# Kernel tuning notes

Measured on AMD Instinct MI355X. Metric: run time of the kernel, lower is better.

## Reference

```python
import jax, jax.numpy as jnp
import numpy as np

N = 50000
NEG_SLOPE = 0.01  # F.leaky_relu default


def gcn_conv(x, edge_index, edge_weight, W, b):
    """PyG GCNConv: h = x @ W; symmetric-normalized aggregation with self-loops; + bias."""
    n = x.shape[0]
    h = x @ W                                # [N, out]
    src, dst = edge_index[0], edge_index[1]
    # degree includes self-loop weight 1.0 per node
    deg = jax.ops.segment_sum(edge_weight, dst, num_segments=n) + 1.0
    dinv = jax.lax.rsqrt(deg)                # deg >= 1, no zero guard needed
    norm = dinv[src] * edge_weight * dinv[dst]
    agg = jax.ops.segment_sum(norm[:, None] * h[src], dst, num_segments=n)
    agg = agg + (dinv * dinv)[:, None] * h   # self-loop contribution: deg^-1 * h_i
    return agg + b


def setup_inputs() -> dict:
    key = jax.random.key(0)
    ks = jax.random.split(key, 24)
    in_size, hid, out = 256, 64, 32
    E = 800000
    d = {}
    for i, nm in enumerate(["x1", "x2", "x3"]):
        d[nm] = jax.random.normal(ks[i], (N, in_size), dtype=jnp.float32)
    for i, nm in enumerate(["edge_index1", "edge_index2", "edge_index3"]):
        d[nm] = jax.random.randint(ks[3 + i], (2, E), 0, N, dtype=jnp.int32)
    for i, nm in enumerate(["edge_weight1", "edge_weight2", "edge_weight3"]):
        d[nm] = jax.random.uniform(ks[6 + i], (E,), dtype=jnp.float32)
    s_in = 1.0 / np.sqrt(in_size)
    s_h = 1.0 / np.sqrt(hid)
    for i, nm in enumerate(["W1", "W2", "W3"]):
        d[nm] = jax.random.uniform(ks[9 + i], (in_size, hid), minval=-s_in, maxval=s_in, dtype=jnp.float32)
    for i, nm in enumerate(["b1", "b2", "b3"]):
        d[nm] = jax.random.uniform(ks[12 + i], (hid,), minval=-s_in, maxval=s_in, dtype=jnp.float32)
    d["fc_w"] = jax.random.uniform(ks[15], (hid, 1), minval=-s_h, maxval=s_h, dtype=jnp.float32)
    d["fc_b"] = jax.random.uniform(ks[16], (1,), minval=-s_h, maxval=s_h, dtype=jnp.float32)
    for i, nm in enumerate(["W11", "W22", "W33"]):
        d[nm] = jax.random.uniform(ks[17 + i], (hid, out), minval=-s_h, maxval=s_h, dtype=jnp.float32)
    for i, nm in enumerate(["b11", "b22", "b33"]):
        d[nm] = jax.random.uniform(ks[20 + i], (out,), minval=-s_h, maxval=s_h, dtype=jnp.float32)
    return d


def reference(x1, x2, x3, edge_index1, edge_index2, edge_index3,
              edge_weight1, edge_weight2, edge_weight3,
              W1, W2, W3, b1, b2, b3, fc_w, fc_b,
              W11, W22, W33, b11, b22, b33):
    # branch embeddings (dropout is identity in eval mode)
    e1 = jax.nn.relu(gcn_conv(x1, edge_index1, edge_weight1, W1, b1))
    e2 = jax.nn.relu(gcn_conv(x2, edge_index2, edge_weight2, W2, b2))
    e3 = jax.nn.relu(gcn_conv(x3, edge_index3, edge_weight3, W3, b3))
    # attention coefficients
    c1 = jnp.exp(jax.nn.leaky_relu(e1 @ fc_w + fc_b, NEG_SLOPE))  # [N,1]
    c2 = jnp.exp(jax.nn.leaky_relu(e2 @ fc_w + fc_b, NEG_SLOPE))
    c3 = jnp.exp(jax.nn.leaky_relu(e3 @ fc_w + fc_b, NEG_SLOPE))
    cd = c1 + c2 + c3
    coef1, coef2, coef3 = c1 / cd, c2 / cd, c3 / cd
    combined = e1 * coef1 + e2 * coef2 + e3 * coef3
    out1 = gcn_conv(combined, edge_index1, edge_weight1, W11, b11)
    out2 = gcn_conv(combined, edge_index2, edge_weight2, W22, b22)
    out3 = gcn_conv(combined, edge_index3, edge_weight3, W33, b33)
    return (out1 + out2 + out3, coef1, coef2, coef3)
```

## Files before the change

### kernel.cpp

```cpp
#include <hip/hip_runtime.h>
#include <hip/hip_fp16.h>
#include <math.h>

#define NN    50000
#define INF_  256
#define HID   64
#define OUTF  32
#define EE    800000
#define TOTN  (3 * NN)
#define NBKT  196
#define NBIN  (3 * NBKT)
#define CBLK  392
#define NCNT  (3 * CBLK)
#define GB    782
#define NGEMM (3 * GB)
#define MAXB  5120
#define NBLK  12500

typedef unsigned long long u64;
typedef unsigned int       u32;
typedef unsigned short     u16;
typedef _Float16           f16;
typedef f16   f16x8 __attribute__((ext_vector_type(8)));
typedef f16   f16x4 __attribute__((ext_vector_type(4)));
typedef float f32x4 __attribute__((ext_vector_type(4)));

__global__ __launch_bounds__(256) void k_prep(
        const float* __restrict__ W1, const float* __restrict__ W2, const float* __restrict__ W3,
        f16* __restrict__ Wt, u32* __restrict__ bin_total) {
    int blk = blockIdx.x, t = threadIdx.x;
    if (blk == 3) {
        for (int i = t; i < NBIN; i += 256) bin_total[i] = 0;
        return;
    }
    const float* W = (blk == 0) ? W1 : (blk == 1) ? W2 : W3;
    f16* wt = Wt + blk * HID * INF_;
    for (int idx = t; idx < INF_ * HID; idx += 256) {
        int k = idx >> 6, c = idx & 63;
        wt[c * INF_ + k] = (f16)W[idx];
    }
}

__global__ __launch_bounds__(256) void k_cntgemm(
        const int* __restrict__ ei1, const int* __restrict__ ei2, const int* __restrict__ ei3,
        u32* __restrict__ bin_total, u32* __restrict__ blockbase,
        const float* __restrict__ x1, const float* __restrict__ x2, const float* __restrict__ x3,
        const f16* __restrict__ Wt, __half* __restrict__ h) {
    __shared__ f16 xl[64][72];
    __shared__ f16 wl[64][72];
    int bid = blockIdx.x;
    int q = bid / 3, r = bid - q * 3;
    int t = threadIdx.x;

    if (r == 2) {
        u32* bins = (u32*)xl;
        int cb  = q;
        int br  = cb / CBLK;
        int blk = cb - br * CBLK;
        const int* ei = (br == 0) ? ei1 : (br == 1) ? ei2 : ei3;
        for (int i = t; i < NBKT; i += 256) bins[i] = 0;
        __syncthreads();
        int e0 = blk * 2048;
#pragma unroll
        for (int k = 0; k < 8; ++k) {
            int e = e0 + k * 256 + t;
            if (e < EE) atomicAdd(&bins[(u32)ei[EE + e] >> 8], 1u);
        }
        __syncthreads();
        for (int i = t; i < NBKT; i += 256) {
            u32 c = bins[i];
            u32 base = atomicAdd(&bin_total[br * NBKT + i], c);
            blockbase[cb * NBKT + i] = base;
        }
        return;
    }

    int gid = q * 2 + r;
    if (gid >= NGEMM) return;
    int b = gid / GB;
    int row_base = (gid - b * GB) * 64;
    const float4* x4 = reinterpret_cast<const float4*>((b == 0) ? x1 : (b == 1) ? x2 : x3);
    const f16* wt = Wt + b * HID * INF_;
    __half* hb = h + (size_t)b * NN * HID;

    int w    = t >> 6;
    int lane = t & 63;
    int lrow = lane & 15;
    int lk   = (lane >> 4) * 8;

    f32x4 acc[4] = {{0,0,0,0},{0,0,0,0},{0,0,0,0},{0,0,0,0}};
    for (int kt = 0; kt < 4; ++kt) {
#pragma unroll
        for (int j = 0; j < 4; ++j) {
            int flat = t + j * 256;
            int rr = flat >> 4, c4 = flat & 15;
            int gr = row_base + rr;
            float4 v = (gr < NN) ? x4[(size_t)gr * 64 + kt * 16 + c4]
                                 : make_float4(0.f, 0.f, 0.f, 0.f);
            f16x4 p = {(f16)v.x, (f16)v.y, (f16)v.z, (f16)v.w};
            *(f16x4*)&xl[rr][c4 * 4] = p;
        }
#pragma unroll
        for (int j = 0; j < 2; ++j) {
            int flat = t + j * 256;
            int col = flat >> 3, ko = (flat & 7) * 8;
            *(f16x8*)&wl[col][ko] = *(const f16x8*)&wt[col * INF_ + kt * 64 + ko];
        }
        __syncthreads();
        int arow = (w << 4) + lrow;
        f16x8 a0 = *(const f16x8*)&xl[arow][lk];
        f16x8 a1 = *(const f16x8*)&xl[arow][32 + lk];
#pragma unroll
        for (int c = 0; c < 4; ++c) {
            f16x8 b0 = *(const f16x8*)&wl[c * 16 + lrow][lk];
            f16x8 b1 = *(const f16x8*)&wl[c * 16 + lrow][32 + lk];
            acc[c] = __builtin_amdgcn_mfma_f32_16x16x32_f16(a0, b0, acc[c], 0, 0, 0);
            acc[c] = __builtin_amdgcn_mfma_f32_16x16x32_f16(a1, b1, acc[c], 0, 0, 0);
        }
        __syncthreads();
    }
    int orow0 = row_base + (w << 4) + ((lane >> 4) << 2);
#pragma unroll
    for (int c = 0; c < 4; ++c) {
#pragma unroll
        for (int i = 0; i < 4; ++i) {
            int row = orow0 + i;
            if (row < NN) hb[(size_t)row * HID + c * 16 + lrow] = __float2half(acc[c][i]);
        }
    }
}

__global__ __launch_bounds__(256) void k_scan(const u32* __restrict__ bin_total,
                                              u32* __restrict__ binstart) {
    __shared__ u32 s[256];
    int t = threadIdx.x;
    u32 c[3]; u32 sum = 0;
#pragma unroll
    for (int k = 0; k < 3; ++k) {
        int i = t * 3 + k;
        c[k] = (i < NBIN) ? bin_total[i] : 0;
        sum += c[k];
    }
    s[t] = sum;
    __syncthreads();
    for (int d = 1; d < 256; d <<= 1) {
        u32 v = (t >= d) ? s[t - d] : 0;
        __syncthreads();
        s[t] += v;
        __syncthreads();
    }
    u32 run = s[t] - sum;
#pragma unroll
    for (int k = 0; k < 3; ++k) {
        int i = t * 3 + k;
        if (i < NBIN) binstart[i] = run;
        run += c[k];
    }
    if (t == 255) binstart[NBIN] = run;
}

__global__ __launch_bounds__(256) void k_scatter(
        const int* __restrict__ ei1, const int* __restrict__ ei2, const int* __restrict__ ei3,
        const float* __restrict__ ew1, const float* __restrict__ ew2, const float* __restrict__ ew3,
        const u32* __restrict__ binstart, const u32* __restrict__ blockbase,
        u64* __restrict__ bucketed) {
    __shared__ u32 cur[NBKT];
    int cb  = blockIdx.x;
    int br  = cb / CBLK;
    int blk = cb - br * CBLK;
    const int*   ei = (br == 0) ? ei1 : (br == 1) ? ei2 : ei3;
    const float* ew = (br == 0) ? ew1 : (br == 1) ? ew2 : ew3;
    int t = threadIdx.x;
    for (int i = t; i < NBKT; i += 256) cur[i] = 0;
    __syncthreads();
    int e0 = blk * 2048;
#pragma unroll
    for (int k = 0; k < 8; ++k) {
        int e = e0 + k * 256 + t;
        if (e < EE) {
            u32 dst = (u32)ei[EE + e];
            u32 src = (u32)ei[e];
            u32 bkt = dst >> 8;
            u32 rnk = atomicAdd(&cur[bkt], 1u);
            u32 pos = binstart[br * NBKT + bkt] + blockbase[cb * NBKT + bkt] + rnk;
            bucketed[pos] = ((u64)__float_as_uint(ew[e]) << 32) | (src << 8) | (dst & 0xffu);
        }
    }
}

__global__ __launch_bounds__(256) void k_bucket(
        const u64* __restrict__ bucketed, const u32* __restrict__ bin_total,
        const u32* __restrict__ binstart,
        u32* __restrict__ nodeinfo, float* __restrict__ dinv,
        u32* __restrict__ csr, __half* __restrict__ h) {
    __shared__ u32   scnt[256];
    __shared__ float swsum[256];
    __shared__ u32   scur[256];
    __shared__ u32   sscan[256];
    __shared__ float sdiv[256];
    __shared__ u32   lcsr[MAXB];
    int bin = blockIdx.x;
    int br  = bin / NBKT;
    int bkt = bin - br * NBKT;
    int t = threadIdx.x;
    u32 base = binstart[bin];
    u32 ecnt = bin_total[bin];
    scnt[t] = 0; swsum[t] = 0.f; scur[t] = 0;
    __syncthreads();
    for (u32 i = t; i < ecnt; i += 256) {
        u64 e = bucketed[base + i];
        u32 dl = (u32)e & 0xffu;
        atomicAdd(&scnt[dl], 1u);
        atomicAdd(&swsum[dl], __uint_as_float((u32)(e >> 32)));
    }
    __syncthreads();
    sscan[t] = scnt[t];
    __syncthreads();
    for (int d = 1; d < 256; d <<= 1) {
        u32 v = (t >= d) ? sscan[t - d] : 0;
        __syncthreads();
        sscan[t] += v;
        __syncthreads();
    }
    u32 lstart = sscan[t] - scnt[t];
    float d = rsqrtf(1.0f + swsum[t]);
    sdiv[t] = d;
    int n = bkt * 256 + t;
    if (n < NN) {
        int gi = br * NN + n;
        nodeinfo[gi] = ((base + lstart) << 10) | scnt[t];
        dinv[gi]     = d;
    }
    __syncthreads();
    for (u32 i = t; i < ecnt; i += 256) {
        u64 e = bucketed[base + i];
        u32 dl  = (u32)e & 0xffu;
        u32 src = (u32)(e >> 8) & 0xffffu;
        float w = __uint_as_float((u32)(e >> 32));
        u32 rnk = atomicAdd(&scur[dl], 1u);
        u32 ls  = sscan[dl] - scnt[dl];
        lcsr[ls + rnk] = ((u32)__half_as_ushort(__float2half(w)) << 16) | src;
    }
    __syncthreads();
    for (u32 i = t; i < ecnt; i += 256) csr[base + i] = lcsr[i];

    int nrows = NN - bkt * 256; if (nrows > 256) nrows = 256;
    u32* hrow = (u32*)(h + ((size_t)br * NN + (size_t)bkt * 256) * HID);
    for (int i = t; i < nrows * 32; i += 256) {
        float dd = sdiv[i >> 5];
        __half2 hv = *(__half2*)&hrow[i];
        float2 v = __half22float2(hv);
        __half2 r = __float22half2_rn(make_float2(v.x * dd, v.y * dd));
        hrow[i] = *(u32*)&r;
    }
}

__global__ __launch_bounds__(256) void k_agg1(
        const u32* __restrict__ csr, const u32* __restrict__ nodeinfo,
        const float* __restrict__ dinv,
        const float* __restrict__ b1, const float* __restrict__ b2, const float* __restrict__ b3,
        const __half* __restrict__ h, __half* __restrict__ e) {
    int bid = blockIdx.x;
    int br  = bid / NBLK;
    int nb  = bid - br * NBLK;
    int t   = threadIdx.x;
    int f2  = t & 31;
    int eo  = (t >> 5) & 1;
    int sub = __builtin_amdgcn_readfirstlane(t >> 6);
    int n   = nb * 4 + sub;

    const float* bi = (br == 0) ? b1 : (br == 1) ? b2 : b3;
    const __half2* hb2 = (const __half2*)(h + (size_t)br * NN * HID);
    int i   = br * NN + n;
    u32 inf = nodeinfo[i];
    int cc  = (int)(inf & 1023u);
    int st  = (int)(inf >> 10);
    float d = dinv[i];
    float2 hs = __half22float2(hb2[(size_t)n * 32 + f2]);

    float ax = 0.f, ay = 0.f;
    int cm1 = cc - 1;
    for (int j = 0; j < cc; j += 16) {
        u32 ee[8]; __half2 vv[8];
#pragma unroll
        for (int u = 0; u < 8; ++u) {
            int jj = j + 2 * u + eo;
            ee[u] = csr[st + (jj < cm1 ? jj : cm1)];
            if (jj >= cc) ee[u] &= 0xffffu;
        }
#pragma unroll
        for (int u = 0; u < 8; ++u)
            vv[u] = hb2[(size_t)(ee[u] & 0xffff) * 32 + f2];
#pragma unroll
        for (int u = 0; u < 8; ++u) {
            float w = __half2float(__ushort_as_half((u16)(ee[u] >> 16)));
            float2 v = __half22float2(vv[u]);
            ax = fmaf(w, v.x, ax);
            ay = fmaf(w, v.y, ay);
        }
    }
    ax += __shfl_xor(ax, 32);
    ay += __shfl_xor(ay, 32);
    float2 bv = ((const float2*)bi)[f2];
    float ex = fmaxf(bv.x + d * (hs.x + ax), 0.f);
    float ey = fmaxf(bv.y + d * (hs.y + ay), 0.f);
    if (eo == 0)
        ((__half2*)e)[((size_t)br * NN + n) * 32 + f2] = __float22half2_rn(make_float2(ex, ey));
}

__global__ __launch_bounds__(256) void k_attn(
        const __half* __restrict__ e,
        const float* __restrict__ fc_w, const float* __restrict__ fc_b,
        __half* __restrict__ comb, float* __restrict__ coef_out) {
    int t    = threadIdx.x;
    int lane = t & 63;
    int sub  = __builtin_amdgcn_readfirstlane(t >> 6);
    int half = lane >> 5;
    int f2   = lane & 31;
    int n    = blockIdx.x * 8 + sub * 2 + half;
    float2 wv = ((const float2*)fc_w)[f2];
    float fb = fc_b[0];
    const __half2* e2 = (const __half2*)e;

    float2 ev[3]; float c[3];
#pragma unroll
    for (int b = 0; b < 3; ++b) {
        ev[b] = __half22float2(e2[((size_t)b * NN + n) * 32 + f2]);
        float dd = ev[b].x * wv.x + ev[b].y * wv.y;
#pragma unroll
        for (int off = 16; off > 0; off >>= 1) dd += __shfl_xor(dd, off);
        float z = dd + fb;
        z = (z > 0.f) ? z : 0.01f * z;
        c[b] = expf(z);
    }
    float cd = c[0] + c[1] + c[2];
    float coef0 = c[0] / cd, coef1 = c[1] / cd, coef2 = c[2] / cd;
    float cx = ev[0].x * coef0 + ev[1].x * coef1 + ev[2].x * coef2;
    float cy = ev[0].y * coef0 + ev[1].y * coef1 + ev[2].y * coef2;
    ((__half2*)comb)[(size_t)n * 32 + f2] = __float22half2_rn(make_float2(cx, cy));
    if (f2 == 0) {
        coef_out[n]          = coef0;
        coef_out[NN + n]     = coef1;
        coef_out[2 * NN + n] = coef2;
    }
}

__global__ __launch_bounds__(256) void k_gemm2(
        const __half* __restrict__ comb,
        const float* __restrict__ W11, const float* __restrict__ W22, const float* __restrict__ W33,
        const float* __restrict__ dinv, __half* __restrict__ h2) {
    __shared__ float Wls[3][HID][OUTF];
    __shared__ __half cl[8][HID];
    int t = threadIdx.x;
    {
        const float4* w40 = reinterpret_cast<const float4*>(W11);
        const float4* w41 = reinterpret_cast<const float4*>(W22);
        const float4* w42 = reinterpret_cast<const float4*>(W33);
        float4* d0 = reinterpret_cast<float4*>(&Wls[0][0][0]);
        float4* d1 = reinterpret_cast<float4*>(&Wls[1][0][0]);
        float4* d2 = reinterpret_cast<float4*>(&Wls[2][0][0]);
#pragma unroll
        for (int j = 0; j < 2; ++j) {
            d0[t + j * 256] = w40[t + j * 256];
            d1[t + j * 256] = w41[t + j * 256];
            d2[t + j * 256] = w42[t + j * 256];
        }
    }
    int row0 = blockIdx.x * 8;
    ((u32*)cl)[t] = ((const u32*)(comb + (size_t)row0 * HID))[t];
    __syncthreads();

    int col = t & 31;
    int rr  = t >> 5;
    int row = row0 + rr;
    float a0 = 0.f, a1 = 0.f, a2 = 0.f;
    for (int k = 0; k < HID; ++k) {
        float cv = __half2float(cl[rr][k]);
        a0 = fmaf(cv, Wls[0][k][col], a0);
        a1 = fmaf(cv, Wls[1][k][col], a1);
        a2 = fmaf(cv, Wls[2][k][col], a2);
    }
    float d0 = dinv[row], d1 = dinv[NN + row], d2 = dinv[2 * NN + row];
    h2[(size_t)0 * NN * OUTF + (size_t)row * OUTF + col] = __float2half(a0 * d0);
    h2[(size_t)1 * NN * OUTF + (size_t)row * OUTF + col] = __float2half(a1 * d1);
    h2[(size_t)2 * NN * OUTF + (size_t)row * OUTF + col] = __float2half(a2 * d2);
}

__global__ __launch_bounds__(256) void k_agg2p(
        const u32* __restrict__ csr, const u32* __restrict__ nodeinfo,
        const float* __restrict__ dinv,
        const __half* __restrict__ h2, float* __restrict__ outp) {
    int bid = blockIdx.x;
    int br  = bid / NBLK;
    int nb  = bid - br * NBLK;
    int t   = threadIdx.x;
    int f2  = t & 15;
    int eo  = (t >> 4) & 3;
    int sub = __builtin_amdgcn_readfirstlane(t >> 6);
    int n   = nb * 4 + sub;

    int i   = br * NN + n;
    u32 inf = nodeinfo[i];
    int cc  = (int)(inf & 1023u);
    int st  = (int)(inf >> 10);
    const __half2* h2b = (const __half2*)(h2 + (size_t)br * NN * OUTF);
    float ax = 0.f, ay = 0.f;
    int cm1 = cc - 1;
    for (int j = 0; j < cc; j += 16) {
        u32 ee[4]; __half2 vv[4];
#pragma unroll
        for (int u = 0; u < 4; ++u) {
            int jj = j + 4 * u + eo;
            ee[u] = csr[st + (jj < cm1 ? jj : cm1)];
            if (jj >= cc) ee[u] &= 0xffffu;
        }
#pragma unroll
        for (int u = 0; u < 4; ++u)
            vv[u] = h2b[(size_t)(ee[u] & 0xffff) * 16 + f2];
#pragma unroll
        for (int u = 0; u < 4; ++u) {
            float w = __half2float(__ushort_as_half((u16)(ee[u] >> 16)));
            float2 v = __half22float2(vv[u]);
            ax = fmaf(w, v.x, ax);
            ay = fmaf(w, v.y, ay);
        }
    }
    ax += __shfl_xor(ax, 16); ay += __shfl_xor(ay, 16);
    ax += __shfl_xor(ax, 32); ay += __shfl_xor(ay, 32);
    float d = dinv[i];
    float2 hs = __half22float2(h2b[(size_t)n * 16 + f2]);
    if (eo == 0)
        ((float2*)outp)[((size_t)br * NN + n) * 16 + f2] =
            make_float2(d * (ax + hs.x), d * (ay + hs.y));
}

__global__ __launch_bounds__(256) void k_sum(
        const float* __restrict__ outp,
        const float* __restrict__ b11, const float* __restrict__ b22, const float* __restrict__ b33,
        float* __restrict__ out) {
    int i = blockIdx.x * 256 + threadIdx.x;
    int f2 = i & 15;
    const float2* p = (const float2*)outp;
    float2 v0 = p[i];
    float2 v1 = p[(size_t)NN * 16 + i];
    float2 v2 = p[(size_t)2 * NN * 16 + i];
    float2 bA = ((const float2*)b11)[f2];
    float2 bB = ((const float2*)b22)[f2];
    float2 bC = ((const float2*)b33)[f2];
    ((float2*)out)[i] = make_float2(v0.x + v1.x + v2.x + bA.x + bB.x + bC.x,
                                    v0.y + v1.y + v2.y + bA.y + bB.y + bC.y);
}

extern "C" void kernel_launch(void* const* d_in, const int* in_sizes, int n_in,
                              void* d_out, int out_size, void* d_ws, size_t ws_size,
                              hipStream_t stream) {
    const float* x1  = (const float*)d_in[0];
    const float* x2  = (const float*)d_in[1];
    const float* x3  = (const float*)d_in[2];
    const int*   ei1 = (const int*)d_in[3];
    const int*   ei2 = (const int*)d_in[4];
    const int*   ei3 = (const int*)d_in[5];
    const float* ew1 = (const float*)d_in[6];
    const float* ew2 = (const float*)d_in[7];
    const float* ew3 = (const float*)d_in[8];
    const float* W1  = (const float*)d_in[9];
    const float* W2  = (const float*)d_in[10];
    const float* W3  = (const float*)d_in[11];
    const float* b1  = (const float*)d_in[12];
    const float* b2  = (const float*)d_in[13];
    const float* b3  = (const float*)d_in[14];
    const float* fcw = (const float*)d_in[15];
    const float* fcb = (const float*)d_in[16];
    const float* W11 = (const float*)d_in[17];
    const float* W22 = (const float*)d_in[18];
    const float* W33 = (const float*)d_in[19];
    const float* b11 = (const float*)d_in[20];
    const float* b22 = (const float*)d_in[21];
    const float* b33 = (const float*)d_in[22];

    float* out = (float*)d_out;
    float* coef_out = out + (size_t)NN * OUTF;

    u64*   bucketed  = (u64*)d_ws;
    float* outp      = (float*)d_ws;
    u32*   csr       = (u32*)(bucketed + 3 * EE);
    u32*   bin_total = csr + 3 * EE;
    u32*   binstart  = bin_total + NBIN;
    u32*   blockbase = binstart + NBIN + 4;
    float* dinv      = (float*)(blockbase + NCNT * NBKT);
    u32*   nodeinfo  = (u32*)(dinv + TOTN);
    f16*   Wt        = (f16*)(nodeinfo + TOTN);
    __half* h        = (__half*)(Wt + 3 * HID * INF_);
    __half* comb     = h + (size_t)TOTN * HID;
    __half* h2       = comb + (size_t)NN * HID;
    __half* e        = h2 + (size_t)TOTN * OUTF;

    k_prep<<<dim3(4), 256, 0, stream>>>(W1, W2, W3, Wt, bin_total);
    k_cntgemm<<<dim3(NCNT * 3), 256, 0, stream>>>(ei1, ei2, ei3, bin_total, blockbase,
                                                  x1, x2, x3, Wt, h);
    k_scan<<<dim3(1), 256, 0, stream>>>(bin_total, binstart);
    k_scatter<<<dim3(NCNT), 256, 0, stream>>>(ei1, ei2, ei3, ew1, ew2, ew3,
                                              binstart, blockbase, bucketed);
    k_bucket<<<dim3(NBIN), 256, 0, stream>>>(bucketed, bin_total, binstart,
                                             nodeinfo, dinv, csr, h);

    k_agg1<<<dim3(3 * NBLK), 256, 0, stream>>>(csr, nodeinfo, dinv, b1, b2, b3, h, e);
    k_attn<<<dim3(NN / 8), 256, 0, stream>>>(e, fcw, fcb, comb, coef_out);
    k_gemm2<<<dim3(NN / 8), 256, 0, stream>>>(comb, W11, W22, W33, dinv, h2);
    k_agg2p<<<dim3(3 * NBLK), 256, 0, stream>>>(csr, nodeinfo, dinv, h2, outp);
    k_sum<<<dim3(3125), 256, 0, stream>>>(outp, b11, b22, b33, out);
}
```

Before: 290.7 us.

## Load GEMM operands directly from global memory into MFMA registers, dropping LDS staging

```diff
diff --git a/kernel.cpp b/kernel.cpp
--- a/kernel.cpp
+++ b/kernel.cpp
@@ -46,14 +46,12 @@
         u32* __restrict__ bin_total, u32* __restrict__ blockbase,
         const float* __restrict__ x1, const float* __restrict__ x2, const float* __restrict__ x3,
         const f16* __restrict__ Wt, __half* __restrict__ h) {
-    __shared__ f16 xl[64][72];
-    __shared__ f16 wl[64][72];
+    __shared__ u32 bins[NBKT];
     int bid = blockIdx.x;
     int q = bid / 3, r = bid - q * 3;
     int t = threadIdx.x;
 
     if (r == 2) {
-        u32* bins = (u32*)xl;
         int cb  = q;
         int br  = cb / CBLK;
         int blk = cb - br * CBLK;
@@ -79,7 +77,7 @@
     if (gid >= NGEMM) return;
     int b = gid / GB;
     int row_base = (gid - b * GB) * 64;
-    const float4* x4 = reinterpret_cast<const float4*>((b == 0) ? x1 : (b == 1) ? x2 : x3);
+    const float* x = (b == 0) ? x1 : (b == 1) ? x2 : x3;
     const f16* wt = Wt + b * HID * INF_;
     __half* hb = h + (size_t)b * NN * HID;
 
@@ -88,36 +86,22 @@
     int lrow = lane & 15;
     int lk   = (lane >> 4) * 8;
 
+    int arow  = row_base + (w << 4) + lrow;
+    int arowc = arow < NN ? arow : NN - 1;
+    const float4* xr = reinterpret_cast<const float4*>(x + (size_t)arowc * INF_);
+
     f32x4 acc[4] = {{0,0,0,0},{0,0,0,0},{0,0,0,0},{0,0,0,0}};
-    for (int kt = 0; kt < 4; ++kt) {
-#pragma unroll
-        for (int j = 0; j < 4; ++j) {
-            int flat = t + j * 256;
-            int rr = flat >> 4, c4 = flat & 15;
-            int gr = row_base + rr;
-            float4 v = (gr < NN) ? x4[(size_t)gr * 64 + kt * 16 + c4]
-                                 : make_float4(0.f, 0.f, 0.f, 0.f);
-            f16x4 p = {(f16)v.x, (f16)v.y, (f16)v.z, (f16)v.w};
-            *(f16x4*)&xl[rr][c4 * 4] = p;
-        }
-#pragma unroll
-        for (int j = 0; j < 2; ++j) {
-            int flat = t + j * 256;
-            int col = flat >> 3, ko = (flat & 7) * 8;
-            *(f16x8*)&wl[col][ko] = *(const f16x8*)&wt[col * INF_ + kt * 64 + ko];
-        }
-        __syncthreads();
-        int arow = (w << 4) + lrow;
-        f16x8 a0 = *(const f16x8*)&xl[arow][lk];
-        f16x8 a1 = *(const f16x8*)&xl[arow][32 + lk];
+#pragma unroll
+    for (int kt = 0; kt < 8; ++kt) {
+        float4 a0 = xr[kt * 8 + (lk >> 2)];
+        float4 a1 = xr[kt * 8 + (lk >> 2) + 1];
+        f16x8 af = {(f16)a0.x, (f16)a0.y, (f16)a0.z, (f16)a0.w,
+                    (f16)a1.x, (f16)a1.y, (f16)a1.z, (f16)a1.w};
 #pragma unroll
         for (int c = 0; c < 4; ++c) {
-            f16x8 b0 = *(const f16x8*)&wl[c * 16 + lrow][lk];
-            f16x8 b1 = *(const f16x8*)&wl[c * 16 + lrow][32 + lk];
-            acc[c] = __builtin_amdgcn_mfma_f32_16x16x32_f16(a0, b0, acc[c], 0, 0, 0);
-            acc[c] = __builtin_amdgcn_mfma_f32_16x16x32_f16(a1, b1, acc[c], 0, 0, 0);
-        }
-        __syncthreads();
+            f16x8 bf = *(const f16x8*)&wt[(c * 16 + lrow) * INF_ + kt * 32 + lk];
+            acc[c] = __builtin_amdgcn_mfma_f32_16x16x32_f16(af, bf, acc[c], 0, 0, 0);
+        }
     }
     int orow0 = row_base + (w << 4) + ((lane >> 4) << 2);
 #pragma unroll
```

New measurement: 319.7 us. 10.0% more time.
